# Kernel tuning notes

Hardware: AMD Instinct MI355X
Metric: run time of the kernel (lower is better)

## Reference

```python
import jax, jax.numpy as jnp
import numpy as np
import math

B, L, D, H = 2, 2048, 1024, 16
HS = D // H  # head size 64


def setup_inputs() -> dict:
    key = jax.random.key(0)
    ks = jax.random.split(key, 4)
    s = 1.0 / math.sqrt(D)
    return {
        "x": jax.random.normal(ks[0], (B, L, D), dtype=jnp.float32),
        "mask": jnp.zeros((B, 1, L, L), dtype=jnp.float32),
        "Wq": jax.random.normal(ks[1], (D, D), dtype=jnp.float32) * s,
        "bq": jnp.zeros((D,), dtype=jnp.float32),
        "Wk": jax.random.normal(ks[2], (D, D), dtype=jnp.float32) * s,
        "bk": jnp.zeros((D,), dtype=jnp.float32),
        "Wv": jax.random.normal(ks[3], (D, D), dtype=jnp.float32) * s,
        "bv": jnp.zeros((D,), dtype=jnp.float32),
    }


def reference(x, mask, Wq, bq, Wk, bk, Wv, bv):
    # projections: torch Linear is x @ W.T + b
    q = (x @ Wq.T + bq).reshape(B, L, H, HS).transpose(0, 2, 1, 3)  # [B,H,L,hs]
    k = (x @ Wk.T + bk).reshape(B, L, H, HS).transpose(0, 2, 1, 3)
    v = (x @ Wv.T + bv).reshape(B, L, H, HS).transpose(0, 2, 1, 3)
    scores = jnp.einsum("bhqd,bhkd->bhqk", q, k) / math.sqrt(HS) + mask
    attn = jax.nn.softmax(scores, axis=-1)  # dropout p=0.0 -> identity
    out = jnp.einsum("bhqk,bhkd->bhqd", attn, v)
    return out.transpose(0, 2, 1, 3).reshape(B, L, D)
```

## Files before the change

kernel.cpp:

```cpp
#include <hip/hip_runtime.h>
#include <cstdint>

#define SEQ 2048
#define DMODEL 1024
#define NHEAD 16
#define HEADSZ 64

typedef __attribute__((ext_vector_type(4))) float f32x4;
typedef __attribute__((ext_vector_type(16))) float f32x16;
typedef __attribute__((ext_vector_type(8))) short short8;
typedef __attribute__((ext_vector_type(4))) unsigned short u16x4;
typedef __attribute__((ext_vector_type(4))) unsigned int u32x4;

#define AS1 __attribute__((address_space(1)))
#define AS3 __attribute__((address_space(3)))

__device__ __forceinline__ void gload_lds16(const void* g, void* l) {
  __builtin_amdgcn_global_load_lds((const AS1 void*)g, (AS3 void*)l, 16, 0, 0);
}

__device__ __forceinline__ unsigned short f2bf(float f) {
  unsigned u = __float_as_uint(f);
  u += 0x7fffu + ((u >> 16) & 1u);
  return (unsigned short)(u >> 16);
}

__device__ __forceinline__ unsigned pack2bf(float lo, float hi) {
  return (unsigned)f2bf(lo) | ((unsigned)f2bf(hi) << 16);
}

__global__ __launch_bounds__(256) void convert_kernel(
    const float* __restrict__ x, const float* __restrict__ wq,
    const float* __restrict__ wk, const float* __restrict__ wv,
    unsigned short* __restrict__ xb, unsigned short* __restrict__ wb) {
  const long i = ((long)blockIdx.x * 256 + threadIdx.x) * 4;
  const float* src;
  unsigned short* dst;
  if (i < (1L << 22)) {
    src = x + i; dst = xb + i;
  } else {
    const long j = i - (1L << 22);
    dst = wb + j;
    if (j < (1L << 20))        src = wq + j;
    else if (j < (2L << 20))   src = wk + (j - (1L << 20));
    else                       src = wv + (j - (2L << 20));
  }
  f32x4 v = *(const f32x4*)src;
  u16x4 o;
  o.x = f2bf(v.x); o.y = f2bf(v.y); o.z = f2bf(v.z); o.w = f2bf(v.w);
  *(u16x4*)dst = o;
}

__global__ __launch_bounds__(256) void qkv_gemm(
    const unsigned short* __restrict__ xb, const unsigned short* __restrict__ wb,
    const float* __restrict__ bq, const float* __restrict__ bk,
    const float* __restrict__ bv,
    unsigned short* __restrict__ qo, unsigned short* __restrict__ ko,
    unsigned short* __restrict__ vto) {
  __shared__ __attribute__((aligned(16))) unsigned short Sh[2][128 * 64];
  unsigned short* As = &Sh[0][0];
  unsigned short* Bs = &Sh[1][0];

  const int bid = blockIdx.x;
  const int swz = (bid & 7) * 96 + (bid >> 3);
  const int tm = swz / 24, tn = swz % 24;
  const int m0 = tm * 128, n0 = tn * 128;
  const int tsel = n0 >> 10;
  const int t = threadIdx.x;
  const int lane = t & 63, wid = t >> 6;
  const int wr = wid >> 1, wc = wid & 1;
  const int r16 = lane & 15, g4 = lane >> 4;

  f32x4 acc[4][4] = {};

  const unsigned short* ga0 = xb + (long)(m0 + (t >> 3)) * 1024 + (t & 7) * 8;
  const unsigned short* gb0 = wb + (long)(n0 + (t >> 3)) * 1024 + (t & 7) * 8;
  char* lA = (char*)As + wid * 1024;
  char* lB = (char*)Bs + wid * 1024;

  for (int ks = 0; ks < 16; ++ks) {
    const unsigned short* ga = ga0 + ks * 64;
    const unsigned short* gb = gb0 + ks * 64;
#pragma unroll
    for (int r = 0; r < 4; ++r) {
      gload_lds16(ga + r * 32 * 1024, lA + r * 4096);
      gload_lds16(gb + r * 32 * 1024, lB + r * 4096);
    }
    __syncthreads();
#pragma unroll
    for (int kk = 0; kk < 2; ++kk) {
      short8 af[4], bf[4];
#pragma unroll
      for (int mi = 0; mi < 4; ++mi)
        af[mi] = *(const short8*)((const char*)As +
                 (wr * 64 + mi * 16 + r16) * 128 + kk * 64 + g4 * 16);
#pragma unroll
      for (int ni = 0; ni < 4; ++ni)
        bf[ni] = *(const short8*)((const char*)Bs +
                 (wc * 64 + ni * 16 + r16) * 128 + kk * 64 + g4 * 16);
      if (tsel < 2) {
#pragma unroll
        for (int mi = 0; mi < 4; ++mi)
#pragma unroll
          for (int ni = 0; ni < 4; ++ni)
            acc[mi][ni] = __builtin_amdgcn_mfma_f32_16x16x32_bf16(
                bf[ni], af[mi], acc[mi][ni], 0, 0, 0);
      } else {
#pragma unroll
        for (int mi = 0; mi < 4; ++mi)
#pragma unroll
          for (int ni = 0; ni < 4; ++ni)
            acc[mi][ni] = __builtin_amdgcn_mfma_f32_16x16x32_bf16(
                af[mi], bf[ni], acc[mi][ni], 0, 0, 0);
      }
    }
    __syncthreads();
  }

  const int bb = m0 >> 11;
  const int lbase = m0 & 2047;
  const int h0n = n0 & 1023;
  unsigned short* T = As;

  if (tsel < 2) {
    const float* bias = tsel == 0 ? bq : bk;
    unsigned short* dst01 = tsel == 0 ? qo : ko;
#pragma unroll
    for (int ni = 0; ni < 4; ++ni) {
      const int nlb = wc * 64 + ni * 16 + g4 * 4;
      const f32x4 b4 = *(const f32x4*)(bias + h0n + nlb);
#pragma unroll
      for (int mi = 0; mi < 4; ++mi) {
        const int ml = wr * 64 + mi * 16 + r16;
        u16x4 pk;
#pragma unroll
        for (int i = 0; i < 4; ++i) pk[i] = f2bf(acc[mi][ni][i] + b4[i]);
        int byteoff = ml * 256 + nlb * 2;
        byteoff ^= (ml & 7) << 4;
        *(u16x4*)((char*)T + byteoff) = pk;
      }
    }
    __syncthreads();
#pragma unroll
    for (int p = 0; p < 8; ++p) {
      const int ml = p * 16 + (t >> 4);
      int byteoff = ml * 256 + ((t & 15) << 4);
      byteoff ^= (ml & 7) << 4;
      short8 row = *(const short8*)((const char*)T + byteoff);
      const int nd = h0n + (t & 15) * 8;
      const int h = nd >> 6, hs = nd & 63;
      *(short8*)(dst01 + ((long)(bb * NHEAD + h) * SEQ + lbase + ml) * 64 + hs) = row;
    }
  } else {
#pragma unroll
    for (int ni = 0; ni < 4; ++ni) {
      const int nl = wc * 64 + ni * 16 + r16;
      const float bval = bv[h0n + nl];
#pragma unroll
      for (int mi = 0; mi < 4; ++mi) {
        const int mlb = wr * 64 + mi * 16 + g4 * 4;
        u16x4 pk;
#pragma unroll
        for (int i = 0; i < 4; ++i) pk[i] = f2bf(acc[mi][ni][i] + bval);
        int byteoff = nl * 256 + mlb * 2;
        byteoff ^= (nl & 7) << 4;
        *(u16x4*)((char*)T + byteoff) = pk;
      }
    }
    __syncthreads();
#pragma unroll
    for (int p = 0; p < 8; ++p) {
      const int nl = p * 16 + (t >> 4);
      int byteoff = nl * 256 + ((t & 15) << 4);
      byteoff ^= (nl & 7) << 4;
      short8 row = *(const short8*)((const char*)T + byteoff);
      const int nd = h0n + nl;
      const int h = nd >> 6, hs = nd & 63;
      *(short8*)(vto + ((((long)(bb * NHEAD + h)) << 6) + hs) * SEQ + lbase +
                 (t & 15) * 8) = row;
    }
  }
}

__global__ __launch_bounds__(256, 2) void attn_kernel(
    const unsigned short* __restrict__ qb, const unsigned short* __restrict__ kb,
    const unsigned short* __restrict__ vtb, const float* __restrict__ mask,
    float* __restrict__ out) {
  __shared__ __attribute__((aligned(16))) char lds[34816];
  unsigned short* Ks = (unsigned short*)lds;
  unsigned short* Vs = (unsigned short*)(lds + 16384);

  const int bid = blockIdx.x;
  const int swz = (bid & 7) * 64 + (bid >> 3);
  const int h = swz & 15, grp = swz >> 4;
  const int qt = grp & 15, b = grp >> 4;
  const int bh = b * NHEAD + h;

  const int t = threadIdx.x;
  const int lane = t & 63, w = t >> 6;
  const int lq = lane & 31;
  const int hi = lane >> 5;

  const unsigned short* qg = qb + (long)bh * SEQ * 64;
  const unsigned short* kg = kb + (long)bh * SEQ * 64;
  const unsigned short* vg = vtb + (long)bh * 64 * SEQ;
  const int q0 = qt * 128 + w * 32;
  const float* mrow = mask + (long)b * SEQ * SEQ + (long)(q0 + lq) * SEQ;

  auto stageKV = [&](int kt, int buf) {
#pragma unroll
    for (int r = 0; r < 2; ++r) {
      const int row = w * 16 + r * 8 + (lane >> 3);
      const int gsw = ((lane & 7) ^ (row & 7)) * 8;
      gload_lds16(kg + (long)(kt * 64 + row) * 64 + gsw,
                  (char*)Ks + buf * 8192 + w * 2048 + r * 1024);
      gload_lds16(vg + (long)row * SEQ + kt * 64 + gsw,
                  (char*)Vs + buf * 8192 + w * 2048 + r * 1024);
    }
  };

  stageKV(0, 0);

  short8 qf[4];
#pragma unroll
  for (int kk = 0; kk < 4; ++kk)
    qf[kk] = *(const short8*)(qg + (long)(q0 + lq) * 64 + hi * 8 + kk * 16);

  f32x16 oa0 = {}, oa1 = {};
  float m_st = -1e30f, l_st = 0.f;

  __syncthreads();

  int cur = 0;
  for (int kt = 0; kt < 32; ++kt) {
    if (kt < 31) stageKV(kt + 1, cur ^ 1);

    const char* Kb = (const char*)Ks + cur * 8192;
    const char* Vb = (const char*)Vs + cur * 8192;

    f32x4 mv[2][4];
#pragma unroll
    for (int k2 = 0; k2 < 2; ++k2)
#pragma unroll
      for (int g = 0; g < 4; ++g)
        mv[k2][g] = *(const f32x4*)(mrow + kt * 64 + k2 * 32 + g * 8 + hi * 4);

    f32x16 sa0 = {}, sa1 = {};
#pragma unroll
    for (int kk = 0; kk < 4; ++kk) {
      const int r0 = lq;
      short8 kf0 = *(const short8*)(Kb + r0 * 128 + (((hi + 2 * kk) ^ (r0 & 7)) << 4));
      sa0 = __builtin_amdgcn_mfma_f32_32x32x16_bf16(kf0, qf[kk], sa0, 0, 0, 0);
      const int r1 = 32 + lq;
      short8 kf1 = *(const short8*)(Kb + r1 * 128 + (((hi + 2 * kk) ^ (r1 & 7)) << 4));
      sa1 = __builtin_amdgcn_mfma_f32_32x32x16_bf16(kf1, qf[kk], sa1, 0, 0, 0);
    }

    float s[32];
#pragma unroll
    for (int r = 0; r < 16; ++r)
      s[r] = sa0[r] * 0.125f + mv[0][r >> 2][r & 3];
#pragma unroll
    for (int r = 0; r < 16; ++r)
      s[16 + r] = sa1[r] * 0.125f + mv[1][r >> 2][r & 3];

    float pm = s[0];
#pragma unroll
    for (int r = 1; r < 32; ++r) pm = fmaxf(pm, s[r]);
    pm = fmaxf(pm, __shfl_xor(pm, 32, 64));
    const float mn = fmaxf(m_st, pm);
    const float alpha = __expf(m_st - mn);
    m_st = mn;

    float rs = 0.f;
#pragma unroll
    for (int r = 0; r < 32; ++r) { s[r] = __expf(s[r] - mn); rs += s[r]; }
    rs += __shfl_xor(rs, 32, 64);
    l_st = l_st * alpha + rs;
#pragma unroll
    for (int r = 0; r < 16; ++r) { oa0[r] *= alpha; oa1[r] *= alpha; }

    u32x4 pw[4];
#pragma unroll
    for (int kk = 0; kk < 4; ++kk) {
      const int base = kk * 8;
      const unsigned X  = pack2bf(s[base + 0], s[base + 1]);
      const unsigned X2 = pack2bf(s[base + 2], s[base + 3]);
      const unsigned Y  = pack2bf(s[base + 4], s[base + 5]);
      const unsigned Y2 = pack2bf(s[base + 6], s[base + 7]);
      const unsigned Xp  = __shfl_xor(X, 32, 64);
      const unsigned X2p = __shfl_xor(X2, 32, 64);
      const unsigned Yp  = __shfl_xor(Y, 32, 64);
      const unsigned Y2p = __shfl_xor(Y2, 32, 64);
      pw[kk][0] = hi ? Yp : X;
      pw[kk][1] = hi ? Y2p : X2;
      pw[kk][2] = hi ? Y : Xp;
      pw[kk][3] = hi ? Y2 : X2p;
    }

#pragma unroll
    for (int kk = 0; kk < 4; ++kk) {
      const short8 pf = __builtin_bit_cast(short8, pw[kk]);
      const int r0 = lq;
      short8 vf0 = *(const short8*)(Vb + r0 * 128 + (((hi + 2 * kk) ^ (r0 & 7)) << 4));
      oa0 = __builtin_amdgcn_mfma_f32_32x32x16_bf16(vf0, pf, oa0, 0, 0, 0);
      const int r1 = 32 + lq;
      short8 vf1 = *(const short8*)(Vb + r1 * 128 + (((hi + 2 * kk) ^ (r1 & 7)) << 4));
      oa1 = __builtin_amdgcn_mfma_f32_32x32x16_bf16(vf1, pf, oa1, 0, 0, 0);
    }

    __syncthreads();
    cur ^= 1;
  }

  __syncthreads();
  float* ot = (float*)lds + w * (32 * 68);
  const float inv_l = 1.f / l_st;
#pragma unroll
  for (int g = 0; g < 4; ++g) {
    f32x4 v0, v1;
#pragma unroll
    for (int j = 0; j < 4; ++j) { v0[j] = oa0[g * 4 + j] * inv_l;
                                  v1[j] = oa1[g * 4 + j] * inv_l; }
    *(f32x4*)(ot + lq * 68 + g * 8 + hi * 4) = v0;
    *(f32x4*)(ot + lq * 68 + 32 + g * 8 + hi * 4) = v1;
  }
  asm volatile("s_waitcnt lgkmcnt(0)" ::: "memory");
  float* ob = out + (long)b * SEQ * DMODEL + (long)q0 * DMODEL + h * 64;
#pragma unroll
  for (int j = 0; j < 8; ++j) {
    const int qr = j * 4 + (lane >> 4);
    f32x4 v4 = *(const f32x4*)(ot + qr * 68 + (lane & 15) * 4);
    *(f32x4*)(ob + (long)qr * DMODEL + (lane & 15) * 4) = v4;
  }
}

extern "C" void kernel_launch(void* const* d_in, const int* in_sizes, int n_in,
                              void* d_out, int out_size, void* d_ws, size_t ws_size,
                              hipStream_t stream) {
  const float* x    = (const float*)d_in[0];
  const float* mask = (const float*)d_in[1];
  const float* Wq   = (const float*)d_in[2];
  const float* bq   = (const float*)d_in[3];
  const float* Wk   = (const float*)d_in[4];
  const float* bk   = (const float*)d_in[5];
  const float* Wv   = (const float*)d_in[6];
  const float* bv   = (const float*)d_in[7];
  float* out = (float*)d_out;

  char* ws = (char*)d_ws;
  unsigned short* xb  = (unsigned short*)(ws);
  unsigned short* wb  = (unsigned short*)(ws + (8L << 20));
  unsigned short* qo  = (unsigned short*)(ws + (14L << 20));
  unsigned short* ko  = (unsigned short*)(ws + (22L << 20));
  unsigned short* vto = (unsigned short*)(ws + (30L << 20));

  convert_kernel<<<7168, 256, 0, stream>>>(x, Wq, Wk, Wv, xb, wb);
  qkv_gemm<<<768, 256, 0, stream>>>(xb, wb, bq, bk, bv, qo, ko, vto);
  attn_kernel<<<512, 256, 0, stream>>>(qo, ko, vto, mask, out);
}
```

Before: 270.1 us.

## Add lazy softmax rescaling, exp2 with folded log2e, split reductions, MFMA priority

The online-softmax running max is now updated only when some lane's new tile max exceeds the stored max by more than a threshold, so the accumulator rescale is skipped on most tiles. Exponentials use exp2f with log2(e) folded into an fma. Max and sum reductions are split into four independent chains to shorten dependency chains. s_setprio raises wave priority around the MFMA blocks to improve interleaving across waves. The lazy rescale allows unnormalized exponentials up to e^8, which is bounded but trades a little fp32/bf16 headroom for fewer multiplies.

```diff
diff --git a/kernel.cpp b/kernel.cpp
--- a/kernel.cpp
+++ b/kernel.cpp
@@ -228,6 +228,7 @@
 
   f32x16 oa0 = {}, oa1 = {};
   float m_st = -1e30f, l_st = 0.f;
+  const float L2E = 1.4426950408889634f;
 
   __syncthreads();
 
@@ -246,6 +247,7 @@
         mv[k2][g] = *(const f32x4*)(mrow + kt * 64 + k2 * 32 + g * 8 + hi * 4);
 
     f32x16 sa0 = {}, sa1 = {};
+    __builtin_amdgcn_s_setprio(1);
 #pragma unroll
     for (int kk = 0; kk < 4; ++kk) {
       const int r0 = lq;
@@ -255,6 +257,7 @@
       short8 kf1 = *(const short8*)(Kb + r1 * 128 + (((hi + 2 * kk) ^ (r1 & 7)) << 4));
       sa1 = __builtin_amdgcn_mfma_f32_32x32x16_bf16(kf1, qf[kk], sa1, 0, 0, 0);
     }
+    __builtin_amdgcn_s_setprio(0);
 
     float s[32];
 #pragma unroll
@@ -264,21 +267,38 @@
     for (int r = 0; r < 16; ++r)
       s[16 + r] = sa1[r] * 0.125f + mv[1][r >> 2][r & 3];
 
-    float pm = s[0];
-#pragma unroll
-    for (int r = 1; r < 32; ++r) pm = fmaxf(pm, s[r]);
+    float pm0 = s[0], pm1 = s[1], pm2 = s[2], pm3 = s[3];
+#pragma unroll
+    for (int r = 4; r < 32; r += 4) {
+      pm0 = fmaxf(pm0, s[r]);     pm1 = fmaxf(pm1, s[r + 1]);
+      pm2 = fmaxf(pm2, s[r + 2]); pm3 = fmaxf(pm3, s[r + 3]);
+    }
+    float pm = fmaxf(fmaxf(pm0, pm1), fmaxf(pm2, pm3));
     pm = fmaxf(pm, __shfl_xor(pm, 32, 64));
-    const float mn = fmaxf(m_st, pm);
-    const float alpha = __expf(m_st - mn);
-    m_st = mn;
-
-    float rs = 0.f;
-#pragma unroll
-    for (int r = 0; r < 32; ++r) { s[r] = __expf(s[r] - mn); rs += s[r]; }
+
+    if (!__all(pm <= m_st + 8.0f)) {
+      const float mn = fmaxf(m_st, pm);
+      const float alpha = exp2f((m_st - mn) * L2E);
+      m_st = mn;
+      l_st *= alpha;
+#pragma unroll
+      for (int r = 0; r < 16; ++r) { oa0[r] *= alpha; oa1[r] *= alpha; }
+    }
+
+    const float nml2e = -m_st * L2E;
+    float rs0 = 0.f, rs1 = 0.f, rs2 = 0.f, rs3 = 0.f;
+#pragma unroll
+    for (int r = 0; r < 32; r += 4) {
+      const float p0 = exp2f(fmaf(s[r], L2E, nml2e));
+      const float p1 = exp2f(fmaf(s[r + 1], L2E, nml2e));
+      const float p2 = exp2f(fmaf(s[r + 2], L2E, nml2e));
+      const float p3 = exp2f(fmaf(s[r + 3], L2E, nml2e));
+      s[r] = p0; s[r + 1] = p1; s[r + 2] = p2; s[r + 3] = p3;
+      rs0 += p0; rs1 += p1; rs2 += p2; rs3 += p3;
+    }
+    float rs = (rs0 + rs1) + (rs2 + rs3);
     rs += __shfl_xor(rs, 32, 64);
-    l_st = l_st * alpha + rs;
-#pragma unroll
-    for (int r = 0; r < 16; ++r) { oa0[r] *= alpha; oa1[r] *= alpha; }
+    l_st += rs;
 
     u32x4 pw[4];
 #pragma unroll
@@ -298,6 +318,7 @@
       pw[kk][3] = hi ? Y2 : X2p;
     }
 
+    __builtin_amdgcn_s_setprio(1);
 #pragma unroll
     for (int kk = 0; kk < 4; ++kk) {
       const short8 pf = __builtin_bit_cast(short8, pw[kk]);
@@ -308,6 +329,7 @@
       short8 vf1 = *(const short8*)(Vb + r1 * 128 + (((hi + 2 * kk) ^ (r1 & 7)) << 4));
       oa1 = __builtin_amdgcn_mfma_f32_32x32x16_bf16(vf1, pf, oa1, 0, 0, 0);
     }
+    __builtin_amdgcn_s_setprio(0);
 
     __syncthreads();
     cur ^= 1;
```

New measurement: 246.9 us. -8.6%, faster.
